# Optimization experiments

Measured on AMD Instinct MI355X. Metric: run time of the kernel, lower is better.

## Reference

```python
import jax, jax.numpy as jnp
import numpy as np
import math

EPS = 1e-5
GROUPS = 32

def group_norm(x, gamma, beta, groups=GROUPS, eps=EPS):
    B, C, H, W = x.shape
    xr = x.reshape(B, groups, C // groups, H, W)
    m = xr.mean(axis=(2, 3, 4), keepdims=True)
    v = xr.var(axis=(2, 3, 4), keepdims=True)
    xr = (xr - m) * jax.lax.rsqrt(v + eps)
    x = xr.reshape(B, C, H, W)
    return x * gamma[None, :, None, None] + beta[None, :, None, None]

def swish(x):
    return x * jax.nn.sigmoid(x)

def conv2d(x, w, b=None, padding='SAME'):
    # x: NCHW, w: OIHW
    y = jax.lax.conv_general_dilated(x, w, window_strides=(1, 1), padding=padding,
                                     dimension_numbers=('NCHW', 'OIHW', 'NCHW'))
    if b is not None:
        y = y + b[None, :, None, None]
    return y

def setup_inputs() -> dict:
    key = jax.random.key(0)
    ks = jax.random.split(key, 24)
    B, C, H, W = 16, 256, 32, 32
    NE = 256  # noise_level_emb_dim
    s = 0.02
    inp = {
        'x': jax.random.normal(ks[0], (B, C, H, W), jnp.float32),
        'time_emb': jax.random.normal(ks[1], (B, NE), jnp.float32),
        'c': jax.random.normal(ks[2], (B, C, H, W), jnp.float32),
        # block1: GroupNorm + Swish + Conv3x3(dim -> dim_out)
        'gn1_g': jnp.ones((C,), jnp.float32),
        'gn1_b': jnp.zeros((C,), jnp.float32),
        'conv1_w': jax.random.normal(ks[3], (C, C, 3, 3), jnp.float32) * s,
        'conv1_b': jnp.zeros((C,), jnp.float32),
        # FeatureWiseAffine linear (use_affine_level=False): Linear(NE -> dim_out)
        'noise_w': jax.random.normal(ks[4], (C, NE), jnp.float32) * s,
        'noise_b': jnp.zeros((C,), jnp.float32),
        # block2: GroupNorm + Swish + Conv3x3(dim_out -> dim_out)
        'gn2_g': jnp.ones((C,), jnp.float32),
        'gn2_b': jnp.zeros((C,), jnp.float32),
        'conv2_w': jax.random.normal(ks[5], (C, C, 3, 3), jnp.float32) * s,
        'conv2_b': jnp.zeros((C,), jnp.float32),
        # c_func: Conv1x1(dim_out -> dim_out)
        'cfunc_w': jax.random.normal(ks[6], (C, C, 1, 1), jnp.float32) * s,
        'cfunc_b': jnp.zeros((C,), jnp.float32),
        # attention: GroupNorm, qkv Conv1x1 (no bias), out Conv1x1
        'attn_gn_g': jnp.ones((C,), jnp.float32),
        'attn_gn_b': jnp.zeros((C,), jnp.float32),
        'qkv_w': jax.random.normal(ks[7], (3 * C, C, 1, 1), jnp.float32) * s,
        'out_w': jax.random.normal(ks[8], (C, C, 1, 1), jnp.float32) * s,
        'out_b': jnp.zeros((C,), jnp.float32),
    }
    return inp

def reference(x, time_emb, c,
              gn1_g, gn1_b, conv1_w, conv1_b,
              noise_w, noise_b,
              gn2_g, gn2_b, conv2_w, conv2_b,
              cfunc_w, cfunc_b,
              attn_gn_g, attn_gn_b, qkv_w, out_w, out_b):
    B, C, H, W = x.shape
    # ---- ResnetBlock ----
    h = conv2d(swish(group_norm(x, gn1_g, gn1_b)), conv1_w, conv1_b)
    # FeatureWiseAffine (additive): h + Linear(time_emb) broadcast over HxW
    h = h + (time_emb @ noise_w.T + noise_b)[:, :, None, None]
    h = conv2d(swish(group_norm(h, gn2_g, gn2_b)), conv2_w, conv2_b)
    h = conv2d(c, cfunc_w, cfunc_b) + h
    h = h + x  # res_conv is Identity since dim == dim_out
    # ---- SelfAttention (n_head=1) ----
    n = group_norm(h, attn_gn_g, attn_gn_b)
    qkv = conv2d(n, qkv_w)                       # [B, 3C, H, W]
    q, k, v = jnp.split(qkv.reshape(B, 3 * C, H * W), 3, axis=1)  # each [B, C, HW]
    scores = jnp.einsum('bcs,bct->bst', q, k) / math.sqrt(C)      # [B, HW, HW]
    attn = jax.nn.softmax(scores, axis=-1)
    o = jnp.einsum('bst,bct->bcs', attn, v).reshape(B, C, H, W)
    o = conv2d(o, out_w, out_b)
    return o + h
```

## Files before the change

### kernel.cpp

```cpp
#include <hip/hip_runtime.h>
#include <hip/hip_bf16.h>
#include <math.h>

typedef __hip_bfloat16 bf16;
typedef short short8 __attribute__((ext_vector_type(8)));
typedef float floatx4 __attribute__((ext_vector_type(4)));

#define NB 16
#define NC 256
#define NHW 1024
#define NNE 256
#define NP (NB*NC*NHW)

__device__ __forceinline__ unsigned short f2bu(float f){
  bf16 h = (bf16)f; return *(unsigned short*)&h;
}

template<bool SWISH>
__global__ void gn_t_kernel(const float* __restrict__ src, const float* __restrict__ gamma,
                            const float* __restrict__ beta, short* __restrict__ xp){
  int b = blockIdx.x >> 5, g = blockIdx.x & 31;
  const int GSZ = 8*NHW;
  size_t base = ((size_t)b*NC + g*8)*NHW;
  int tid = threadIdx.x;
  float s = 0.f, ss = 0.f;
  for (int i = tid; i < GSZ; i += 256){
    float v = src[base+i];
    s += v; ss += v*v;
  }
  __shared__ float rs[256], rq[256];
  rs[tid] = s; rq[tid] = ss;
  __syncthreads();
  for (int off=128; off>0; off>>=1){
    if (tid < off){ rs[tid]+=rs[tid+off]; rq[tid]+=rq[tid+off]; }
    __syncthreads();
  }
  float mean = rs[0] * (1.f/GSZ);
  float var  = rq[0] * (1.f/GSZ) - mean*mean;
  float inv  = rsqrtf(var + 1e-5f);
  float gm[8], bt[8];
  #pragma unroll
  for (int j=0;j<8;j++){ gm[j] = gamma[g*8+j]*inv; bt[j] = beta[g*8+j]; }
  short* dst = xp + (((size_t)b*8 + (g>>2))*NHW)*32 + (g&3)*8;
  for (int px = tid; px < NHW; px += 256){
    short8 pk;
    #pragma unroll
    for (int j=0;j<8;j++){
      float v = (src[base + j*NHW + px] - mean)*gm[j] + bt[j];
      if (SWISH) v = v / (1.f + __expf(-v));
      pk[j] = (short)f2bu(v);
    }
    *(short8*)(dst + (size_t)px*32) = pk;
  }
}

template<bool SWISH>
__global__ void gn_post_kernel(const float* __restrict__ src, const float* __restrict__ st,
                               const float* __restrict__ gamma, const float* __restrict__ beta,
                               short* __restrict__ xp){
  int b = blockIdx.x >> 5, g = blockIdx.x & 31;
  size_t base = ((size_t)b*NC + g*8)*NHW;
  int tid = threadIdx.x;
  float s  = st[(b*32+g)*2+0];
  float ss = st[(b*32+g)*2+1];
  float mean = s * (1.f/8192.f);
  float var  = ss * (1.f/8192.f) - mean*mean;
  float inv  = rsqrtf(var + 1e-5f);
  float gm[8], bt[8];
  #pragma unroll
  for (int j=0;j<8;j++){ gm[j] = gamma[g*8+j]*inv; bt[j] = beta[g*8+j]; }
  short* dst = xp + (((size_t)b*8 + (g>>2))*NHW)*32 + (g&3)*8;
  for (int px = tid; px < NHW; px += 256){
    short8 pk;
    #pragma unroll
    for (int j=0;j<8;j++){
      float v = (src[base + j*NHW + px] - mean)*gm[j] + bt[j];
      if (SWISH) v = v / (1.f + __expf(-v));
      pk[j] = (short)f2bu(v);
    }
    *(short8*)(dst + (size_t)px*32) = pk;
  }
}

__global__ void wprep3_kernel(const float* __restrict__ w1, const float* __restrict__ w2,
                              short* __restrict__ wp1, short* __restrict__ wp2,
                              float* __restrict__ st){
  int co = blockIdx.x & 255;
  const float* w = (blockIdx.x < 256) ? w1 : w2;
  short* wp = (blockIdx.x < 256) ? wp1 : wp2;
  int tid = threadIdx.x;
  if (blockIdx.x == 0){
    for (int i=tid;i<2048;i+=256) st[i] = 0.f;
  }
  __shared__ float tmp[2304];
  for (int i=tid;i<2304;i+=256) tmp[i] = w[(size_t)co*2304 + i];
  __syncthreads();
  for (int j=tid;j<2304;j+=256){
    int tap = j>>8, ci = j&255;
    wp[(((size_t)tap*8 + (ci>>5))*NC + co)*32 + (ci&31)] = (short)f2bu(tmp[ci*9 + tap]);
  }
}

__global__ void wprep1_kernel(const float* __restrict__ wq, const float* __restrict__ wc,
                              const float* __restrict__ wo,
                              short* __restrict__ wqp, short* __restrict__ wcp,
                              short* __restrict__ wop){
  int blk = blockIdx.x, tid = threadIdx.x;
  if (blk < 768){
    float v = wq[(size_t)blk*256 + tid];
    wqp[(((size_t)(tid>>5))*768 + blk)*32 + (tid&31)] = (short)f2bu(v);
  } else if (blk < 1024){
    int co = blk - 768;
    float v = wc[(size_t)co*256 + tid];
    wcp[(((size_t)(tid>>5))*256 + co)*32 + (tid&31)] = (short)f2bu(v);
  } else {
    int co = blk - 1024;
    float v = wo[(size_t)co*256 + tid];
    wop[(((size_t)(tid>>5))*256 + co)*32 + (tid&31)] = (short)f2bu(v);
  }
}

__global__ void cvtc_kernel(const float* __restrict__ c_in, short* __restrict__ cp){
  int pxc = blockIdx.x, cc = blockIdx.y, b = blockIdx.z, tid = threadIdx.x;
  __shared__ float ld[32][257];
  size_t gbase = ((size_t)b*NC + cc*32)*NHW + pxc*256;
  for (int j=0;j<32;j++) ld[j][tid] = c_in[gbase + (size_t)j*NHW + tid];
  __syncthreads();
  short* dst = cp + (((size_t)b*8 + cc)*NHW + pxc*256)*32;
  for (int it=0;it<4;it++){
    int pxl = it*64 + (tid>>2), ckl = tid&3;
    short8 pk;
    #pragma unroll
    for (int e=0;e<8;e++) pk[e] = (short)f2bu(ld[ckl*8+e][pxl]);
    *(short8*)(dst + (size_t)pxl*32 + ckl*8) = pk;
  }
}

__global__ void noise_kernel(const float* __restrict__ emb, const float* __restrict__ w,
                             const float* __restrict__ bias, float* __restrict__ na){
  int b = blockIdx.x, c = threadIdx.x;
  __shared__ float e[NNE];
  e[c] = emb[b*NNE + c];
  __syncthreads();
  float acc = bias[c];
  for (int k=0;k<NNE;k++) acc += e[k]*w[c*NNE+k];
  na[b*NC + c] = acc;
}

#define XSTR 264
__global__ __launch_bounds__(256,1)
void conv3_mfma_kernel(const short* __restrict__ xp, const short* __restrict__ wp,
                       const float* __restrict__ bias, const float* __restrict__ bias_bc,
                       const float* __restrict__ addf, float* __restrict__ out,
                       float* __restrict__ st){
  const int b = blockIdx.y, y0 = blockIdx.x*2;
  const int tid = threadIdx.x, wave = tid>>6, lane = tid&63;
  const int quad = lane>>4, lm = lane&15;
  __shared__ short Xs[4*34*XSTR];

  {
    int r = tid>>6, side = (tid>>5)&1, ck = tid&31;
    short8 z = {0,0,0,0,0,0,0,0};
    *(short8*)&Xs[((r*34) + side*33)*XSTR + ck*8] = z;
  }
  for (int it=0; it<16; ++it){
    int idx = it*256 + tid;
    int r = idx>>10, rem = idx&1023;
    int cc = rem>>7, x = (rem>>2)&31, ckl = rem&3;
    int y = y0 - 1 + r;
    short8 v = {0,0,0,0,0,0,0,0};
    if ((unsigned)y < 32u)
      v = *(const short8*)(xp + (((size_t)b*8 + cc)*NHW + y*32 + x)*32 + ckl*8);
    *(short8*)&Xs[(r*34 + x + 1)*XSTR + (cc*4 + ckl)*8] = v;
  }
  __syncthreads();

  floatx4 acc[4][4];
  #pragma unroll
  for (int mt=0;mt<4;mt++)
    #pragma unroll
    for (int nt=0;nt<4;nt++) acc[mt][nt] = (floatx4){0.f,0.f,0.f,0.f};

  const int co_w = wave*64;
  const int aoff = (co_w + lm)*32 + quad*8;

  auto ldA = [&](int j, short8 a[4]){
    const short* p = wp + (size_t)j*NC*32 + aoff;
    #pragma unroll
    for (int mt=0;mt<4;mt++) a[mt] = *(const short8*)(p + mt*(16*32));
  };
  auto ldB = [&](int j, short8 bf[4]){
    int tap = j>>3, kk = j&7;
    int dy = (tap*11)>>5;
    int dxp = tap - dy*3;
    int base = (lm+dxp)*XSTR + quad*8 + kk*32 + dy*(34*XSTR);
    #pragma unroll
    for (int nt=0;nt<4;nt++)
      bf[nt] = *(const short8*)&Xs[base + (nt>>1)*(34*XSTR) + (nt&1)*(16*XSTR)];
  };

  short8 A[4][4], Bf[4][4];
  ldA(0,A[0]); ldB(0,Bf[0]);
  ldA(1,A[1]); ldB(1,Bf[1]);
  ldA(2,A[2]); ldB(2,Bf[2]);
  ldA(3,A[3]); ldB(3,Bf[3]);
  for (int it=0; it<72; it+=4){
    #pragma unroll
    for (int u=0;u<4;u++){
      #pragma unroll
      for (int mt=0;mt<4;mt++)
        #pragma unroll
        for (int nt=0;nt<4;nt++)
          acc[mt][nt] = __builtin_amdgcn_mfma_f32_16x16x32_bf16(A[u][mt], Bf[u][nt], acc[mt][nt], 0,0,0);
      int j = it + 4 + u; if (j > 71) j = 71;
      ldA(j, A[u]); ldB(j, Bf[u]);
    }
  }

  const int hw0 = blockIdx.x*64;
  float gs[4], gq[4];
  #pragma unroll
  for (int mt=0;mt<4;mt++){ gs[mt]=0.f; gq[mt]=0.f; }
  #pragma unroll
  for (int mt=0;mt<4;mt++){
    #pragma unroll
    for (int r=0;r<4;r++){
      int co = co_w + mt*16 + quad*4 + r;
      float bb = bias[co] + (bias_bc ? bias_bc[b*NC + co] : 0.f);
      size_t ob = ((size_t)b*NC + co)*NHW + hw0;
      #pragma unroll
      for (int nt=0;nt<4;nt++){
        size_t oi = ob + nt*16 + lm;
        float v = acc[mt][nt][r] + bb;
        if (addf) v += addf[oi];
        out[oi] = v;
        gs[mt] += v; gq[mt] += v*v;
      }
    }
  }
  #pragma unroll
  for (int mt=0;mt<4;mt++){
    float s = gs[mt], q = gq[mt];
    #pragma unroll
    for (int o=1;o<32;o<<=1){ s += __shfl_xor(s, o, 64); q += __shfl_xor(q, o, 64); }
    if ((lane&31) == 0){
      int g = (co_w>>3) + mt*2 + (quad>>1);
      atomicAdd(&st[(b*32+g)*2+0], s);
      atomicAdd(&st[(b*32+g)*2+1], q);
    }
  }
}

__global__ __launch_bounds__(256)
void gemm_cfunc_kernel(const short* __restrict__ cp, const short* __restrict__ wcp,
                       const float* __restrict__ bias, const float* __restrict__ xres,
                       float* __restrict__ out){
  const int b = blockIdx.z;
  const int tid = threadIdx.x, wave = tid>>6, lane = tid&63;
  const int quad = lane>>4, lm = lane&15;
  const int M0 = blockIdx.y*128 + (wave>>1)*64;
  const int N0 = blockIdx.x*128 + (wave&1)*64;
  floatx4 acc[4][4];
  #pragma unroll
  for (int mt=0;mt<4;mt++)
    #pragma unroll
    for (int nt=0;nt<4;nt++) acc[mt][nt] = (floatx4){0.f,0.f,0.f,0.f};
  #pragma unroll
  for (int kk=0;kk<8;kk++){
    short8 af[4], bfr[4];
    #pragma unroll
    for (int mt=0;mt<4;mt++)
      af[mt] = *(const short8*)(wcp + ((size_t)kk*256 + M0 + mt*16 + lm)*32 + quad*8);
    #pragma unroll
    for (int nt=0;nt<4;nt++)
      bfr[nt] = *(const short8*)(cp + (((size_t)b*8 + kk)*NHW + N0 + nt*16 + lm)*32 + quad*8);
    #pragma unroll
    for (int mt=0;mt<4;mt++)
      #pragma unroll
      for (int nt=0;nt<4;nt++)
        acc[mt][nt] = __builtin_amdgcn_mfma_f32_16x16x32_bf16(af[mt], bfr[nt], acc[mt][nt], 0,0,0);
  }
  #pragma unroll
  for (int mt=0;mt<4;mt++){
    #pragma unroll
    for (int r=0;r<4;r++){
      int co = M0 + mt*16 + quad*4 + r;
      float bb = bias[co];
      size_t ob = ((size_t)b*NC + co)*NHW + N0;
      #pragma unroll
      for (int nt=0;nt<4;nt++){
        size_t oi = ob + nt*16 + lm;
        out[oi] = acc[mt][nt][r] + bb + xres[oi];
      }
    }
  }
}

__global__ __launch_bounds__(256)
void gemm_qkv_kernel(const short* __restrict__ ntp, const short* __restrict__ wqp,
                     short* __restrict__ qp, short* __restrict__ kp, short* __restrict__ vp){
  const int b = blockIdx.z;
  const int tid = threadIdx.x, wave = tid>>6, lane = tid&63;
  const int quad = lane>>4, lm = lane&15;
  const int M0 = blockIdx.y*128 + (wave>>1)*64;
  const int N0 = blockIdx.x*128 + (wave&1)*64;
  floatx4 acc[4][4];
  #pragma unroll
  for (int mt=0;mt<4;mt++)
    #pragma unroll
    for (int nt=0;nt<4;nt++) acc[mt][nt] = (floatx4){0.f,0.f,0.f,0.f};
  #pragma unroll
  for (int kk=0;kk<8;kk++){
    short8 af[4], bfr[4];
    #pragma unroll
    for (int mt=0;mt<4;mt++)
      af[mt] = *(const short8*)(wqp + ((size_t)kk*768 + M0 + mt*16 + lm)*32 + quad*8);
    #pragma unroll
    for (int nt=0;nt<4;nt++)
      bfr[nt] = *(const short8*)(ntp + (((size_t)b*8 + kk)*NHW + N0 + nt*16 + lm)*32 + quad*8);
    #pragma unroll
    for (int mt=0;mt<4;mt++)
      #pragma unroll
      for (int nt=0;nt<4;nt++)
        acc[mt][nt] = __builtin_amdgcn_mfma_f32_16x16x32_bf16(af[mt], bfr[nt], acc[mt][nt], 0,0,0);
  }
  #pragma unroll
  for (int mt=0;mt<4;mt++){
    int co_base = M0 + mt*16 + quad*4;
    int sec = co_base >> 8;
    int c = co_base & 255;
    #pragma unroll
    for (int nt=0;nt<4;nt++){
      int s = N0 + nt*16 + lm;
      if (sec < 2){
        unsigned short t0 = f2bu(acc[mt][nt][0]), t1 = f2bu(acc[mt][nt][1]);
        unsigned short t2 = f2bu(acc[mt][nt][2]), t3 = f2bu(acc[mt][nt][3]);
        uint2 w2; w2.x = ((unsigned)t1<<16)|t0; w2.y = ((unsigned)t3<<16)|t2;
        short* dst = (sec==0) ? qp : kp;
        *(uint2*)(dst + (((size_t)b*8 + (c>>5))*NHW + s)*32 + (c&31)) = w2;
      } else {
        #pragma unroll
        for (int r=0;r<4;r++)
          vp[(((size_t)b*32 + (s>>5))*NC + c + r)*32 + (s&31)] = (short)f2bu(acc[mt][nt][r]);
      }
    }
  }
}

__global__ __launch_bounds__(256)
void attn_mfma_kernel(const short* __restrict__ qp, const short* __restrict__ kp,
                      const short* __restrict__ vp, short* __restrict__ op){
  const int bx = blockIdx.x;
  const int b = bx & 15;
  const int s0 = (bx >> 4) * 16;
  const int tid = threadIdx.x, wave = tid>>6, lane = tid&63;
  const int quad = lane>>4, lm = lane&15;
  __shared__ short P[16][1032];
  __shared__ float redmax[16][4], redsum[16][4];

  short8 aq[8];
  #pragma unroll
  for (int kk=0;kk<8;kk++)
    aq[kk] = *(const short8*)(qp + (((size_t)b*8 + kk)*NHW + s0 + lm)*32 + quad*8);

  floatx4 sc[16];
  #pragma unroll
  for (int ti=0;ti<16;ti++) sc[ti] = (floatx4){0.f,0.f,0.f,0.f};

  const int trow0 = wave*256 + lm;
  short8 kf[3][4];
  #pragma unroll
  for (int g=0;g<3;g++)
    #pragma unroll
    for (int j=0;j<4;j++)
      kf[g][j] = *(const short8*)(kp + (((size_t)b*8 + (g&1)*4 + j)*NHW + trow0 + (g>>1)*16)*32 + quad*8);
  #pragma unroll
  for (int g=0;g<32;g++){
    const int u = g%3, ti = g>>1, h = g&1;
    #pragma unroll
    for (int j=0;j<4;j++)
      sc[ti] = __builtin_amdgcn_mfma_f32_16x16x32_bf16(aq[h*4+j], kf[u][j], sc[ti], 0,0,0);
    if (g < 29){
      const int gn = g+3, tin = gn>>1, hn = gn&1;
      #pragma unroll
      for (int j=0;j<4;j++)
        kf[u][j] = *(const short8*)(kp + (((size_t)b*8 + hn*4 + j)*NHW + trow0 + tin*16)*32 + quad*8);
    }
  }

  const float scale = 0.0625f;
  float mx[4] = {-1e30f,-1e30f,-1e30f,-1e30f};
  #pragma unroll
  for (int ti=0;ti<16;ti++)
    #pragma unroll
    for (int r=0;r<4;r++){
      float v = sc[ti][r]*scale;
      sc[ti][r] = v;
      mx[r] = fmaxf(mx[r], v);
    }
  #pragma unroll
  for (int o=1;o<16;o<<=1)
    #pragma unroll
    for (int r=0;r<4;r++) mx[r] = fmaxf(mx[r], __shfl_xor(mx[r], o, 64));
  if (lm==0){
    #pragma unroll
    for (int r=0;r<4;r++) redmax[quad*4+r][wave] = mx[r];
  }
  __syncthreads();
  float fm[4];
  #pragma unroll
  for (int r=0;r<4;r++){
    int row = quad*4+r;
    fm[r] = fmaxf(fmaxf(redmax[row][0],redmax[row][1]),
                  fmaxf(redmax[row][2],redmax[row][3]));
  }
  float sm[4] = {0.f,0.f,0.f,0.f};
  #pragma unroll
  for (int ti=0;ti<16;ti++)
    #pragma unroll
    for (int r=0;r<4;r++){
      float e = __expf(sc[ti][r] - fm[r]);
      sc[ti][r] = e;
      sm[r] += e;
    }
  #pragma unroll
  for (int o=1;o<16;o<<=1)
    #pragma unroll
    for (int r=0;r<4;r++) sm[r] += __shfl_xor(sm[r], o, 64);
  if (lm==0){
    #pragma unroll
    for (int r=0;r<4;r++) redsum[quad*4+r][wave] = sm[r];
  }
  __syncthreads();
  float inv[4];
  #pragma unroll
  for (int r=0;r<4;r++){
    int row = quad*4+r;
    inv[r] = 1.f/(redsum[row][0]+redsum[row][1]+redsum[row][2]+redsum[row][3]);
  }
  #pragma unroll
  for (int ti=0;ti<16;ti++)
    #pragma unroll
    for (int r=0;r<4;r++)
      P[quad*4+r][wave*256 + ti*16 + lm] = (short)f2bu(sc[ti][r]*inv[r]);
  __syncthreads();

  floatx4 oacc[4];
  #pragma unroll
  for (int nt=0;nt<4;nt++) oacc[nt] = (floatx4){0.f,0.f,0.f,0.f};
  const int crow = wave*64 + lm;
  short8 vf[3][4], pf[3];
  #pragma unroll
  for (int u=0;u<3;u++){
    pf[u] = *(const short8*)(&P[lm][u*32 + quad*8]);
    #pragma unroll
    for (int nt=0;nt<4;nt++)
      vf[u][nt] = *(const short8*)(vp + (((size_t)b*32 + u)*NC + crow + nt*16)*32 + quad*8);
  }
  #pragma unroll
  for (int kk=0;kk<32;kk++){
    const int u = kk%3;
    #pragma unroll
    for (int nt=0;nt<4;nt++)
      oacc[nt] = __builtin_amdgcn_mfma_f32_16x16x32_bf16(pf[u], vf[u][nt], oacc[nt], 0,0,0);
    if (kk < 29){
      pf[u] = *(const short8*)(&P[lm][(kk+3)*32 + quad*8]);
      #pragma unroll
      for (int nt=0;nt<4;nt++)
        vf[u][nt] = *(const short8*)(vp + (((size_t)b*32 + kk+3)*NC + crow + nt*16)*32 + quad*8);
    }
  }
  #pragma unroll
  for (int nt=0;nt<4;nt++){
    int c = wave*64 + nt*16 + lm;
    int cc = c>>5, cl = c&31;
    #pragma unroll
    for (int r=0;r<4;r++){
      int s = s0 + quad*4 + r;
      op[(((size_t)b*8 + cc)*NHW + s)*32 + cl] = (short)f2bu(oacc[nt][r]);
    }
  }
}

__global__ __launch_bounds__(256)
void outproj_mfma_kernel(const short* __restrict__ op, const short* __restrict__ wop,
                         const float* __restrict__ obias, const float* __restrict__ h,
                         float* __restrict__ out){
  const int b = blockIdx.z;
  const int tid = threadIdx.x, wave = tid>>6, lane = tid&63;
  const int quad = lane>>4, lm = lane&15;
  const int M0 = blockIdx.y*128 + (wave>>1)*64;
  const int N0 = blockIdx.x*128 + (wave&1)*64;
  floatx4 acc[4][4];
  #pragma unroll
  for (int mt=0;mt<4;mt++)
    #pragma unroll
    for (int nt=0;nt<4;nt++) acc[mt][nt] = (floatx4){0.f,0.f,0.f,0.f};
  #pragma unroll
  for (int kk=0;kk<8;kk++){
    short8 af[4], bfr[4];
    #pragma unroll
    for (int mt=0;mt<4;mt++)
      af[mt] = *(const short8*)(wop + ((size_t)kk*256 + M0 + mt*16 + lm)*32 + quad*8);
    #pragma unroll
    for (int nt=0;nt<4;nt++)
      bfr[nt] = *(const short8*)(op + (((size_t)b*8 + kk)*NHW + N0 + nt*16 + lm)*32 + quad*8);
    #pragma unroll
    for (int mt=0;mt<4;mt++)
      #pragma unroll
      for (int nt=0;nt<4;nt++)
        acc[mt][nt] = __builtin_amdgcn_mfma_f32_16x16x32_bf16(af[mt], bfr[nt], acc[mt][nt], 0,0,0);
  }
  #pragma unroll
  for (int mt=0;mt<4;mt++){
    #pragma unroll
    for (int r=0;r<4;r++){
      int co = M0 + mt*16 + quad*4 + r;
      float bb = obias[co];
      size_t ob = ((size_t)b*NC + co)*NHW + N0;
      #pragma unroll
      for (int nt=0;nt<4;nt++){
        size_t oi = ob + nt*16 + lm;
        out[oi] = acc[mt][nt][r] + bb + h[oi];
      }
    }
  }
}

extern "C" void kernel_launch(void* const* d_in, const int* in_sizes, int n_in,
                              void* d_out, int out_size, void* d_ws, size_t ws_size,
                              hipStream_t stream){
  const float* x        = (const float*)d_in[0];
  const float* time_emb = (const float*)d_in[1];
  const float* c_in     = (const float*)d_in[2];
  const float* gn1_g    = (const float*)d_in[3];
  const float* gn1_b    = (const float*)d_in[4];
  const float* conv1_w  = (const float*)d_in[5];
  const float* conv1_b  = (const float*)d_in[6];
  const float* noise_w  = (const float*)d_in[7];
  const float* noise_b  = (const float*)d_in[8];
  const float* gn2_g    = (const float*)d_in[9];
  const float* gn2_b    = (const float*)d_in[10];
  const float* conv2_w  = (const float*)d_in[11];
  const float* conv2_b  = (const float*)d_in[12];
  const float* cfunc_w  = (const float*)d_in[13];
  const float* cfunc_b  = (const float*)d_in[14];
  const float* agn_g    = (const float*)d_in[15];
  const float* agn_b    = (const float*)d_in[16];
  const float* qkv_w    = (const float*)d_in[17];
  const float* out_w    = (const float*)d_in[18];
  const float* out_b    = (const float*)d_in[19];
  float* outp = (float*)d_out;

  float* ws = (float*)d_ws;
  float* buf_h = ws;
  float* buf_t = buf_h + NP;
  short* xpb   = (short*)(buf_t + NP);
  short* qp    = xpb + NP;
  short* kp    = qp + NP;
  short* vp    = kp + NP;
  short* wp1   = vp + NP;
  short* wp2   = wp1 + 589824;
  short* wqp   = wp2 + 589824;
  short* wcp   = wqp + 196608;
  short* wop   = wcp + 65536;
  float* na    = (float*)(wop + 65536);
  float* st    = na + NB*NC;
  float* st2   = st;
  float* st3   = st + 1024;
  short* cp    = (short*)buf_t;
  short* op    = (short*)buf_t;

  wprep3_kernel<<<512, 256, 0, stream>>>(conv1_w, conv2_w, wp1, wp2, st);
  wprep1_kernel<<<1280, 256, 0, stream>>>(qkv_w, cfunc_w, out_w, wqp, wcp, wop);
  cvtc_kernel<<<dim3(4,8,NB), 256, 0, stream>>>(c_in, cp);
  noise_kernel<<<NB, 256, 0, stream>>>(time_emb, noise_w, noise_b, na);
  gn_t_kernel<true><<<NB*32, 256, 0, stream>>>(x, gn1_g, gn1_b, xpb);
  conv3_mfma_kernel<<<dim3(16, NB), 256, 0, stream>>>(xpb, wp1, conv1_b, na, nullptr, buf_h, st2);
  gn_post_kernel<true><<<NB*32, 256, 0, stream>>>(buf_h, st2, gn2_g, gn2_b, xpb);
  gemm_cfunc_kernel<<<dim3(8,2,NB), 256, 0, stream>>>(cp, wcp, cfunc_b, x, buf_h);
  conv3_mfma_kernel<<<dim3(16, NB), 256, 0, stream>>>(xpb, wp2, conv2_b, nullptr, buf_h, buf_h, st3);
  gn_post_kernel<false><<<NB*32, 256, 0, stream>>>(buf_h, st3, agn_g, agn_b, xpb);
  gemm_qkv_kernel<<<dim3(8,6,NB), 256, 0, stream>>>(xpb, wqp, qp, kp, vp);
  attn_mfma_kernel<<<1024, 256, 0, stream>>>(qp, kp, vp, op);
  outproj_mfma_kernel<<<dim3(8,2,NB), 256, 0, stream>>>(op, wop, out_b, buf_h, outp);
}
```

Measured before the change: 375.5 us.

## Process 32 query rows per attention block to reuse K and V fragments

```diff
diff --git a/kernel.cpp b/kernel.cpp
--- a/kernel.cpp
+++ b/kernel.cpp
@@ -352,36 +352,42 @@
                       const short* __restrict__ vp, short* __restrict__ op){
   const int bx = blockIdx.x;
   const int b = bx & 15;
-  const int s0 = (bx >> 4) * 16;
+  const int s0 = (bx >> 4) * 32;
   const int tid = threadIdx.x, wave = tid>>6, lane = tid&63;
   const int quad = lane>>4, lm = lane&15;
-  __shared__ short P[16][1032];
-  __shared__ float redmax[16][4], redsum[16][4];
-
-  short8 aq[8];
-  #pragma unroll
-  for (int kk=0;kk<8;kk++)
-    aq[kk] = *(const short8*)(qp + (((size_t)b*8 + kk)*NHW + s0 + lm)*32 + quad*8);
-
-  floatx4 sc[16];
-  #pragma unroll
-  for (int ti=0;ti<16;ti++) sc[ti] = (floatx4){0.f,0.f,0.f,0.f};
+  __shared__ short P[32][1032];
+  __shared__ float redmax[32][4], redsum[32][4];
+
+  short8 aq[2][8];
+  #pragma unroll
+  for (int m=0;m<2;m++)
+    #pragma unroll
+    for (int kk=0;kk<8;kk++)
+      aq[m][kk] = *(const short8*)(qp + (((size_t)b*8 + kk)*NHW + s0 + m*16 + lm)*32 + quad*8);
+
+  floatx4 sc[2][16];
+  #pragma unroll
+  for (int m=0;m<2;m++)
+    #pragma unroll
+    for (int ti=0;ti<16;ti++) sc[m][ti] = (floatx4){0.f,0.f,0.f,0.f};
 
   const int trow0 = wave*256 + lm;
-  short8 kf[3][4];
-  #pragma unroll
-  for (int g=0;g<3;g++)
+  short8 kf[2][4];
+  #pragma unroll
+  for (int u=0;u<2;u++)
     #pragma unroll
     for (int j=0;j<4;j++)
-      kf[g][j] = *(const short8*)(kp + (((size_t)b*8 + (g&1)*4 + j)*NHW + trow0 + (g>>1)*16)*32 + quad*8);
+      kf[u][j] = *(const short8*)(kp + (((size_t)b*8 + (u&1)*4 + j)*NHW + trow0 + (u>>1)*16)*32 + quad*8);
   #pragma unroll
   for (int g=0;g<32;g++){
-    const int u = g%3, ti = g>>1, h = g&1;
-    #pragma unroll
-    for (int j=0;j<4;j++)
-      sc[ti] = __builtin_amdgcn_mfma_f32_16x16x32_bf16(aq[h*4+j], kf[u][j], sc[ti], 0,0,0);
-    if (g < 29){
-      const int gn = g+3, tin = gn>>1, hn = gn&1;
+    const int u = g&1, ti = g>>1, h = g&1;
+    #pragma unroll
+    for (int j=0;j<4;j++){
+      sc[0][ti] = __builtin_amdgcn_mfma_f32_16x16x32_bf16(aq[0][h*4+j], kf[u][j], sc[0][ti], 0,0,0);
+      sc[1][ti] = __builtin_amdgcn_mfma_f32_16x16x32_bf16(aq[1][h*4+j], kf[u][j], sc[1][ti], 0,0,0);
+    }
+    if (g < 30){
+      const int gn = g+2, tin = gn>>1, hn = gn&1;
       #pragma unroll
       for (int j=0;j<4;j++)
         kf[u][j] = *(const short8*)(kp + (((size_t)b*8 + hn*4 + j)*NHW + trow0 + tin*16)*32 + quad*8);
@@ -389,85 +395,119 @@
   }
 
   const float scale = 0.0625f;
-  float mx[4] = {-1e30f,-1e30f,-1e30f,-1e30f};
-  #pragma unroll
-  for (int ti=0;ti<16;ti++)
+  float mx[2][4];
+  #pragma unroll
+  for (int m=0;m<2;m++)
+    #pragma unroll
+    for (int r=0;r<4;r++) mx[m][r] = -1e30f;
+  #pragma unroll
+  for (int m=0;m<2;m++)
+    #pragma unroll
+    for (int ti=0;ti<16;ti++)
+      #pragma unroll
+      for (int r=0;r<4;r++){
+        float v = sc[m][ti][r]*scale;
+        sc[m][ti][r] = v;
+        mx[m][r] = fmaxf(mx[m][r], v);
+      }
+  #pragma unroll
+  for (int o=1;o<16;o<<=1)
+    #pragma unroll
+    for (int m=0;m<2;m++)
+      #pragma unroll
+      for (int r=0;r<4;r++) mx[m][r] = fmaxf(mx[m][r], __shfl_xor(mx[m][r], o, 64));
+  if (lm==0){
+    #pragma unroll
+    for (int m=0;m<2;m++)
+      #pragma unroll
+      for (int r=0;r<4;r++) redmax[m*16 + quad*4 + r][wave] = mx[m][r];
+  }
+  __syncthreads();
+  float fm[2][4];
+  #pragma unroll
+  for (int m=0;m<2;m++)
     #pragma unroll
     for (int r=0;r<4;r++){
-      float v = sc[ti][r]*scale;
-      sc[ti][r] = v;
-      mx[r] = fmaxf(mx[r], v);
-    }
+      int row = m*16 + quad*4 + r;
+      fm[m][r] = fmaxf(fmaxf(redmax[row][0],redmax[row][1]),
+                       fmaxf(redmax[row][2],redmax[row][3]));
+    }
+  float sm[2][4];
+  #pragma unroll
+  for (int m=0;m<2;m++)
+    #pragma unroll
+    for (int r=0;r<4;r++) sm[m][r] = 0.f;
+  #pragma unroll
+  for (int m=0;m<2;m++)
+    #pragma unroll
+    for (int ti=0;ti<16;ti++)
+      #pragma unroll
+      for (int r=0;r<4;r++){
+        float e = __expf(sc[m][ti][r] - fm[m][r]);
+        sc[m][ti][r] = e;
+        sm[m][r] += e;
+      }
   #pragma unroll
   for (int o=1;o<16;o<<=1)
     #pragma unroll
-    for (int r=0;r<4;r++) mx[r] = fmaxf(mx[r], __shfl_xor(mx[r], o, 64));
+    for (int m=0;m<2;m++)
+      #pragma unroll
+      for (int r=0;r<4;r++) sm[m][r] += __shfl_xor(sm[m][r], o, 64);
   if (lm==0){
     #pragma unroll
-    for (int r=0;r<4;r++) redmax[quad*4+r][wave] = mx[r];
-  }
-  __syncthreads();
-  float fm[4];
-  #pragma unroll
-  for (int r=0;r<4;r++){
-    int row = quad*4+r;
-    fm[r] = fmaxf(fmaxf(redmax[row][0],redmax[row][1]),
-                  fmaxf(redmax[row][2],redmax[row][3]));
-  }
-  float sm[4] = {0.f,0.f,0.f,0.f};
-  #pragma unroll
-  for (int ti=0;ti<16;ti++)
+    for (int m=0;m<2;m++)
+      #pragma unroll
+      for (int r=0;r<4;r++) redsum[m*16 + quad*4 + r][wave] = sm[m][r];
+  }
+  __syncthreads();
+  float inv[2][4];
+  #pragma unroll
+  for (int m=0;m<2;m++)
     #pragma unroll
     for (int r=0;r<4;r++){
-      float e = __expf(sc[ti][r] - fm[r]);
-      sc[ti][r] = e;
-      sm[r] += e;
-    }
-  #pragma unroll
-  for (int o=1;o<16;o<<=1)
-    #pragma unroll
-    for (int r=0;r<4;r++) sm[r] += __shfl_xor(sm[r], o, 64);
-  if (lm==0){
-    #pragma unroll
-    for (int r=0;r<4;r++) redsum[quad*4+r][wave] = sm[r];
-  }
-  __syncthreads();
-  float inv[4];
-  #pragma unroll
-  for (int r=0;r<4;r++){
-    int row = quad*4+r;
-    inv[r] = 1.f/(redsum[row][0]+redsum[row][1]+redsum[row][2]+redsum[row][3]);
-  }
-  #pragma unroll
-  for (int ti=0;ti<16;ti++)
-    #pragma unroll
-    for (int r=0;r<4;r++)
-      P[quad*4+r][wave*256 + ti*16 + lm] = (short)f2bu(sc[ti][r]*inv[r]);
-  __syncthreads();
-
-  floatx4 oacc[4];
-  #pragma unroll
-  for (int nt=0;nt<4;nt++) oacc[nt] = (floatx4){0.f,0.f,0.f,0.f};
+      int row = m*16 + quad*4 + r;
+      inv[m][r] = 1.f/(redsum[row][0]+redsum[row][1]+redsum[row][2]+redsum[row][3]);
+    }
+  #pragma unroll
+  for (int m=0;m<2;m++)
+    #pragma unroll
+    for (int ti=0;ti<16;ti++)
+      #pragma unroll
+      for (int r=0;r<4;r++)
+        P[m*16 + quad*4 + r][wave*256 + ti*16 + lm] = (short)f2bu(sc[m][ti][r]*inv[m][r]);
+  __syncthreads();
+
+  floatx4 oacc[2][4];
+  #pragma unroll
+  for (int m=0;m<2;m++)
+    #pragma unroll
+    for (int nt=0;nt<4;nt++) oacc[m][nt] = (floatx4){0.f,0.f,0.f,0.f};
   const int crow = wave*64 + lm;
-  short8 vf[3][4], pf[3];
-  #pragma unroll
-  for (int u=0;u<3;u++){
-    pf[u] = *(const short8*)(&P[lm][u*32 + quad*8]);
+  short8 vf[2][4], pf[2][2];
+  #pragma unroll
+  for (int u=0;u<2;u++){
+    #pragma unroll
+    for (int m=0;m<2;m++)
+      pf[u][m] = *(const short8*)(&P[m*16 + lm][u*32 + quad*8]);
     #pragma unroll
     for (int nt=0;nt<4;nt++)
       vf[u][nt] = *(const short8*)(vp + (((size_t)b*32 + u)*NC + crow + nt*16)*32 + quad*8);
   }
   #pragma unroll
   for (int kk=0;kk<32;kk++){
-    const int u = kk%3;
-    #pragma unroll
-    for (int nt=0;nt<4;nt++)
-      oacc[nt] = __builtin_amdgcn_mfma_f32_16x16x32_bf16(pf[u], vf[u][nt], oacc[nt], 0,0,0);
-    if (kk < 29){
-      pf[u] = *(const short8*)(&P[lm][(kk+3)*32 + quad*8]);
+    const int u = kk&1;
+    #pragma unroll
+    for (int nt=0;nt<4;nt++){
+      oacc[0][nt] = __builtin_amdgcn_mfma_f32_16x16x32_bf16(pf[u][0], vf[u][nt], oacc[0][nt], 0,0,0);
+      oacc[1][nt] = __builtin_amdgcn_mfma_f32_16x16x32_bf16(pf[u][1], vf[u][nt], oacc[1][nt], 0,0,0);
+    }
+    if (kk < 30){
+      #pragma unroll
+      for (int m=0;m<2;m++)
+        pf[u][m] = *(const short8*)(&P[m*16 + lm][(kk+2)*32 + quad*8]);
       #pragma unroll
       for (int nt=0;nt<4;nt++)
-        vf[u][nt] = *(const short8*)(vp + (((size_t)b*32 + kk+3)*NC + crow + nt*16)*32 + quad*8);
+        vf[u][nt] = *(const short8*)(vp + (((size_t)b*32 + kk+2)*NC + crow + nt*16)*32 + quad*8);
     }
   }
   #pragma unroll
@@ -475,10 +515,12 @@
     int c = wave*64 + nt*16 + lm;
     int cc = c>>5, cl = c&31;
     #pragma unroll
-    for (int r=0;r<4;r++){
-      int s = s0 + quad*4 + r;
-      op[(((size_t)b*8 + cc)*NHW + s)*32 + cl] = (short)f2bu(oacc[nt][r]);
-    }
+    for (int m=0;m<2;m++)
+      #pragma unroll
+      for (int r=0;r<4;r++){
+        int s = s0 + m*16 + quad*4 + r;
+        op[(((size_t)b*8 + cc)*NHW + s)*32 + cl] = (short)f2bu(oacc[m][nt][r]);
+      }
   }
 }
 
@@ -582,6 +624,6 @@
   conv3_mfma_kernel<<<dim3(16, NB), 256, 0, stream>>>(xpb, wp2, conv2_b, nullptr, buf_h, buf_h, st3);
   gn_post_kernel<false><<<NB*32, 256, 0, stream>>>(buf_h, st3, agn_g, agn_b, xpb);
   gemm_qkv_kernel<<<dim3(8,6,NB), 256, 0, stream>>>(xpb, wqp, qp, kp, vp);
-  attn_mfma_kernel<<<1024, 256, 0, stream>>>(qp, kp, vp, op);
+  attn_mfma_kernel<<<512, 256, 0, stream>>>(qp, kp, vp, op);
   outproj_mfma_kernel<<<dim3(8,2,NB), 256, 0, stream>>>(op, wop, out_b, buf_h, outp);
 }
```

New measurement: 373.5 us. Within noise of the previous version (-0.5%).
